# Kernel optimization log

Hardware: AMD Instinct MI355X
Metric: run time of the kernel (lower is better)

## Reference

```python
import jax, jax.numpy as jnp
import numpy as np


def setup_inputs() -> dict:
    key = jax.random.key(0)
    k1, k2 = jax.random.split(key)
    X = jax.random.normal(k1, (8192, 3), dtype=jnp.float32)
    Y = jax.random.normal(k2, (8192, 3), dtype=jnp.float32)
    return {"X": X, "Y": Y}


def reference(X, Y):
    # Pairwise L2 distances: torch.norm(x - y) for every (x, y) pair.
    # d[i, j] = ||X[i] - Y[j]||_2, shape [N, M]
    diff = X[:, None, :] - Y[None, :, :]          # [N, M, D]
    d = jnp.sqrt(jnp.sum(diff * diff, axis=-1))   # [N, M]
    hd_xy = jnp.max(jnp.min(d, axis=1))           # max over x of min over y
    hd_yx = jnp.max(jnp.min(d, axis=0))           # max over y of min over x
    return jnp.maximum(hd_xy, hd_yx)
```

## Files before the change

### kernel.cpp

```cpp
#include <hip/hip_runtime.h>
#include <math.h>


typedef float v2f __attribute__((ext_vector_type(2)));

constexpr int NPTS = 8192;
constexpr int T = 256;
constexpr int R = 8;
constexpr int ROWS_PB = T * R;
constexpr int RG = NPTS / ROWS_PB;
constexpr int CG = 64;
constexpr int COLS = NPTS / CG;

__global__ __launch_bounds__(T) void pair_partial_kernel(
        const float* __restrict__ X, const float* __restrict__ Y,
        float* __restrict__ partial) {
    int b = blockIdx.x;
    int dir = b / (RG * CG);
    int rem = b - dir * (RG * CG);
    int rg = rem / CG;
    int cg = rem - rg * CG;
    const float* A = dir ? Y : X;
    const float* B = dir ? X : Y;

    int t = threadIdx.x;
    int r0 = rg * ROWS_PB + t;

    float ax[R], ay[R], az[R];
#pragma unroll
    for (int k = 0; k < R; ++k) {
        int row = r0 + k * T;
        ax[k] = A[row * 3 + 0];
        ay[k] = A[row * 3 + 1];
        az[k] = A[row * 3 + 2];
    }

    __shared__ float4 Bs[COLS];
    for (int i = t; i < COLS; i += T) {
        int j = cg * COLS + i;
        float bx = B[j * 3 + 0], by = B[j * 3 + 1], bz = B[j * 3 + 2];
        Bs[i] = make_float4(bx, by, bz, -0.5f * fmaf(bx, bx, fmaf(by, by, bz * bz)));
    }

    v2f ax2[R / 2], ay2[R / 2], az2[R / 2], na2[R / 2], mt2[R / 2];
#pragma unroll
    for (int q = 0; q < R / 2; ++q) {
        ax2[q] = (v2f){ax[2 * q], ax[2 * q + 1]};
        ay2[q] = (v2f){ay[2 * q], ay[2 * q + 1]};
        az2[q] = (v2f){az[2 * q], az[2 * q + 1]};
        na2[q] = ax2[q] * ax2[q] + ay2[q] * ay2[q] + az2[q] * az2[q];
        mt2[q] = (v2f){-__builtin_inff(), -__builtin_inff()};
    }
    __syncthreads();

#pragma unroll 8
    for (int j = 0; j < COLS; ++j) {
        float4 p = Bs[j];
        v2f px = (v2f){p.x, p.x};
        v2f py = (v2f){p.y, p.y};
        v2f pz = (v2f){p.z, p.z};
        v2f pw = (v2f){p.w, p.w};
#pragma unroll
        for (int q = 0; q < R / 2; ++q) {
            v2f tt = az2[q] * pz + pw;
            tt = ay2[q] * py + tt;
            tt = ax2[q] * px + tt;
            mt2[q].x = fmaxf(mt2[q].x, tt.x);
            mt2[q].y = fmaxf(mt2[q].y, tt.y);
        }
    }

    float* op = partial + (size_t)(dir * CG + cg) * NPTS + rg * ROWS_PB + t;
#pragma unroll
    for (int q = 0; q < R / 2; ++q) {
        op[(2 * q) * T]     = fmaf(-2.f, mt2[q].x, na2[q].x);
        op[(2 * q + 1) * T] = fmaf(-2.f, mt2[q].y, na2[q].y);
    }
}

template <int CGN>
__global__ __launch_bounds__(T) void reduce_kernel(
        const float* __restrict__ partial, float* __restrict__ blockmax) {
    int rid = blockIdx.x * T + threadIdx.x;
    int dir = rid >> 13;
    int row = rid & (NPTS - 1);
    const float* p = partial + (size_t)dir * CGN * NPTS + row;
    float m0 = __builtin_inff(), m1 = __builtin_inff();
#pragma unroll 8
    for (int cg = 0; cg < CGN; cg += 2) {
        m0 = fminf(m0, p[(size_t)cg * NPTS]);
        m1 = fminf(m1, p[(size_t)(cg + 1) * NPTS]);
    }
    float m = fmaxf(fminf(m0, m1), 0.f);
    for (int o = 32; o > 0; o >>= 1) m = fmaxf(m, __shfl_down(m, o));
    __shared__ float wm[T / 64];
    if ((threadIdx.x & 63) == 0) wm[threadIdx.x >> 6] = m;
    __syncthreads();
    if (threadIdx.x == 0) {
        float mm = wm[0];
        for (int w = 1; w < T / 64; ++w) mm = fmaxf(mm, wm[w]);
        blockmax[blockIdx.x] = mm;
    }
}

__global__ void final_kernel(const float* __restrict__ blockmax,
                             float* __restrict__ out, int n) {
    float m = blockmax[threadIdx.x < n ? threadIdx.x : 0];
    for (int o = 32; o > 0; o >>= 1) m = fmaxf(m, __shfl_down(m, o));
    if (threadIdx.x == 0) out[0] = sqrtf(m);
}


constexpr int SEG_J = 512;
constexpr int SEGS = NPTS / SEG_J;

__global__ void init_min_kernel(unsigned* wsmin, int n) {
    int i = blockIdx.x * blockDim.x + threadIdx.x;
    if (i < n) wsmin[i] = 0x7F800000u;
}

__global__ __launch_bounds__(T) void pair_min_kernel(
        const float* __restrict__ X, const float* __restrict__ Y,
        unsigned* __restrict__ minXY, unsigned* __restrict__ minYX) {
    constexpr int RPB = T * 8;
    constexpr int BLOCKS_PER_DIR = (NPTS / RPB) * SEGS;
    int b = blockIdx.x;
    int dir = b / BLOCKS_PER_DIR;
    int rem = b - dir * BLOCKS_PER_DIR;
    int rg = rem / SEGS;
    int seg = rem - rg * SEGS;
    const float* A = dir ? Y : X;
    const float* B = dir ? X : Y;
    unsigned* omin = dir ? minYX : minXY;

    __shared__ float Bs[SEG_J * 3];
    int t = threadIdx.x;
    const float* Bseg = B + seg * SEG_J * 3;
    for (int i = t; i < SEG_J * 3; i += T) Bs[i] = Bseg[i];

    int r0 = rg * RPB + t;
    float ax[8], ay[8], az[8], m[8];
#pragma unroll
    for (int r = 0; r < 8; ++r) {
        int row = r0 + r * T;
        ax[r] = A[row * 3 + 0];
        ay[r] = A[row * 3 + 1];
        az[r] = A[row * 3 + 2];
        m[r] = __builtin_inff();
    }
    __syncthreads();

#pragma unroll 2
    for (int j = 0; j < SEG_J; ++j) {
        float bx = Bs[3 * j + 0], by = Bs[3 * j + 1], bz = Bs[3 * j + 2];
#pragma unroll
        for (int r = 0; r < 8; ++r) {
            float dx = ax[r] - bx, dy = ay[r] - by, dz = az[r] - bz;
            m[r] = fminf(m[r], fmaf(dx, dx, fmaf(dy, dy, dz * dz)));
        }
    }
#pragma unroll
    for (int r = 0; r < 8; ++r)
        atomicMin(&omin[r0 + r * T], __float_as_uint(m[r]));
}

__global__ __launch_bounds__(T) void finalize_min_kernel(
        const unsigned* __restrict__ wsmin, float* __restrict__ out, int n) {
    int t = threadIdx.x;
    float mx = 0.f;
    for (int i = t; i < n; i += T) mx = fmaxf(mx, __uint_as_float(wsmin[i]));
    for (int o = 32; o > 0; o >>= 1) mx = fmaxf(mx, __shfl_down(mx, o));
    __shared__ float wmax[T / 64];
    if ((t & 63) == 0) wmax[t >> 6] = mx;
    __syncthreads();
    if (t == 0) {
        float mm = wmax[0];
        for (int w = 1; w < T / 64; ++w) mm = fmaxf(mm, wmax[w]);
        out[0] = sqrtf(mm);
    }
}

extern "C" void kernel_launch(void* const* d_in, const int* in_sizes, int n_in,
                              void* d_out, int out_size, void* d_ws, size_t ws_size,
                              hipStream_t stream) {
    const float* X = (const float*)d_in[0];
    const float* Y = (const float*)d_in[1];
    float* out = (float*)d_out;

    const size_t need = (size_t)(2 * CG * NPTS + 2 * NPTS / T) * sizeof(float);

    if (ws_size >= need) {
        float* partial = (float*)d_ws;
        float* blockmax = partial + 2 * CG * NPTS;
        pair_partial_kernel<<<2 * RG * CG, T, 0, stream>>>(X, Y, partial);
        reduce_kernel<CG><<<2 * NPTS / T, T, 0, stream>>>(partial, blockmax);
        final_kernel<<<1, 64, 0, stream>>>(blockmax, out, 2 * NPTS / T);
    } else if (ws_size >= 2 * NPTS * sizeof(unsigned)) {
        unsigned* wsmin = (unsigned*)d_ws;
        init_min_kernel<<<(2 * NPTS + T - 1) / T, T, 0, stream>>>(wsmin, 2 * NPTS);
        pair_min_kernel<<<2 * (NPTS / (T * 8)) * SEGS, T, 0, stream>>>(
            X, Y, wsmin, wsmin + NPTS);
        finalize_min_kernel<<<1, T, 0, stream>>>(wsmin, out, 2 * NPTS);
    }
}
```

Before: 25.86 us.

## Fuse partial-min, reduction and final max into one kernel with atomics

Replaces the per-column-group partial buffer and two follow-up reduction kernels with atomicMin on a per-row buffer, plus a last-block-done counter that does the final max and sqrt inside the main kernel. This removes the large partial write and read and two kernel launches. In exchange it adds two memset launches, contended atomics (64 per row address), and a serial final scan of 16K values by a single block. The buffer is memset to 0x7F7F7F7F, a large finite float rather than infinity, which works as an initial minimum.

```diff
diff --git a/kernel.cpp b/kernel.cpp
--- a/kernel.cpp
+++ b/kernel.cpp
@@ -11,10 +11,13 @@
 constexpr int RG = NPTS / ROWS_PB;
 constexpr int CG = 64;
 constexpr int COLS = NPTS / CG;
-
-__global__ __launch_bounds__(T) void pair_partial_kernel(
+constexpr int NBLK = 2 * RG * CG;
+
+__global__ __launch_bounds__(T) void hausdorff_fused_kernel(
         const float* __restrict__ X, const float* __restrict__ Y,
-        float* __restrict__ partial) {
+        unsigned* __restrict__ minbuf,
+        unsigned* __restrict__ counter,
+        float* __restrict__ out) {
     int b = blockIdx.x;
     int dir = b / (RG * CG);
     int rem = b - dir * (RG * CG);
@@ -70,44 +73,37 @@
         }
     }
 
-    float* op = partial + (size_t)(dir * CG + cg) * NPTS + rg * ROWS_PB + t;
+    unsigned* om = minbuf + dir * NPTS + rg * ROWS_PB + t;
 #pragma unroll
     for (int q = 0; q < R / 2; ++q) {
-        op[(2 * q) * T]     = fmaf(-2.f, mt2[q].x, na2[q].x);
-        op[(2 * q + 1) * T] = fmaf(-2.f, mt2[q].y, na2[q].y);
-    }
-}
-
-template <int CGN>
-__global__ __launch_bounds__(T) void reduce_kernel(
-        const float* __restrict__ partial, float* __restrict__ blockmax) {
-    int rid = blockIdx.x * T + threadIdx.x;
-    int dir = rid >> 13;
-    int row = rid & (NPTS - 1);
-    const float* p = partial + (size_t)dir * CGN * NPTS + row;
-    float m0 = __builtin_inff(), m1 = __builtin_inff();
-#pragma unroll 8
-    for (int cg = 0; cg < CGN; cg += 2) {
-        m0 = fminf(m0, p[(size_t)cg * NPTS]);
-        m1 = fminf(m1, p[(size_t)(cg + 1) * NPTS]);
-    }
-    float m = fmaxf(fminf(m0, m1), 0.f);
-    for (int o = 32; o > 0; o >>= 1) m = fmaxf(m, __shfl_down(m, o));
+        float d0 = fmaxf(fmaf(-2.f, mt2[q].x, na2[q].x), 0.f);
+        float d1 = fmaxf(fmaf(-2.f, mt2[q].y, na2[q].y), 0.f);
+        atomicMin(&om[(2 * q) * T], __float_as_uint(d0));
+        atomicMin(&om[(2 * q + 1) * T], __float_as_uint(d1));
+    }
+
+    __threadfence();
+    __shared__ unsigned is_last;
+    if (t == 0) is_last = (atomicAdd(counter, 1u) == NBLK - 1) ? 1u : 0u;
+    __syncthreads();
+    if (!is_last) return;
+
+    __threadfence();
+    float mx = 0.f;
+    for (int i = t; i < 2 * NPTS; i += T) {
+        unsigned u = __hip_atomic_load(&minbuf[i], __ATOMIC_RELAXED,
+                                       __HIP_MEMORY_SCOPE_AGENT);
+        mx = fmaxf(mx, __uint_as_float(u));
+    }
+    for (int o = 32; o > 0; o >>= 1) mx = fmaxf(mx, __shfl_down(mx, o));
     __shared__ float wm[T / 64];
-    if ((threadIdx.x & 63) == 0) wm[threadIdx.x >> 6] = m;
-    __syncthreads();
-    if (threadIdx.x == 0) {
+    if ((t & 63) == 0) wm[t >> 6] = mx;
+    __syncthreads();
+    if (t == 0) {
         float mm = wm[0];
         for (int w = 1; w < T / 64; ++w) mm = fmaxf(mm, wm[w]);
-        blockmax[blockIdx.x] = mm;
-    }
-}
-
-__global__ void final_kernel(const float* __restrict__ blockmax,
-                             float* __restrict__ out, int n) {
-    float m = blockmax[threadIdx.x < n ? threadIdx.x : 0];
-    for (int o = 32; o > 0; o >>= 1) m = fmaxf(m, __shfl_down(m, o));
-    if (threadIdx.x == 0) out[0] = sqrtf(m);
+        out[0] = sqrtf(mm);
+    }
 }
 
 
@@ -187,15 +183,15 @@
     const float* Y = (const float*)d_in[1];
     float* out = (float*)d_out;
 
-    const size_t need = (size_t)(2 * CG * NPTS + 2 * NPTS / T) * sizeof(float);
-
-    if (ws_size >= need) {
-        float* partial = (float*)d_ws;
-        float* blockmax = partial + 2 * CG * NPTS;
-        pair_partial_kernel<<<2 * RG * CG, T, 0, stream>>>(X, Y, partial);
-        reduce_kernel<CG><<<2 * NPTS / T, T, 0, stream>>>(partial, blockmax);
-        final_kernel<<<1, 64, 0, stream>>>(blockmax, out, 2 * NPTS / T);
-    } else if (ws_size >= 2 * NPTS * sizeof(unsigned)) {
+    const size_t minbuf_bytes = (size_t)2 * NPTS * sizeof(unsigned);
+
+    if (ws_size >= minbuf_bytes + sizeof(unsigned)) {
+        unsigned* minbuf = (unsigned*)d_ws;
+        unsigned* counter = (unsigned*)((char*)d_ws + minbuf_bytes);
+        hipMemsetAsync(minbuf, 0x7F, minbuf_bytes, stream);
+        hipMemsetAsync(counter, 0, sizeof(unsigned), stream);
+        hausdorff_fused_kernel<<<NBLK, T, 0, stream>>>(X, Y, minbuf, counter, out);
+    } else if (ws_size >= minbuf_bytes) {
         unsigned* wsmin = (unsigned*)d_ws;
         init_min_kernel<<<(2 * NPTS + T - 1) / T, T, 0, stream>>>(wsmin, 2 * NPTS);
         pair_min_kernel<<<2 * (NPTS / (T * 8)) * SEGS, T, 0, stream>>>(
```

Result: slower. 65.04 us (+151.5%).
